# Kernel optimization log

Hardware: AMD Instinct MI355X
Metric: run time of the kernel (lower is better)

## Reference

```python
import jax, jax.numpy as jnp
import numpy as np

HEAD = 32  # HEAD_SIZE
B, T, C = 8, 1024, 768
LAYER_ID, N_LAYER = 2, 12


def wkv7(r, w, k, v, a, b):
    # RWKV7 linear recurrence (matches the custom CUDA 'attn' kernel math):
    #   S = S * exp(-exp(w)) + (S @ a) b^T + v k^T ;  y = S @ r
    Bb, Tt, Cc = r.shape
    H, N = Cc // HEAD, HEAD
    rs = lambda z: jnp.moveaxis(z.reshape(Bb, Tt, H, N), 1, 0)  # [T,B,H,N]
    rT, kT, vT, aT, bT = rs(r), rs(k), rs(v), rs(a), rs(b)
    wT = rs(jnp.exp(-jnp.exp(w)))  # decay in (0,1)
    def step(S, inp):
        rt, wt, kt, vt, at, bt = inp  # each [B,H,N]
        sa = jnp.einsum('bhij,bhj->bhi', S, at)
        S = S * wt[:, :, None, :] + sa[..., None] * bt[:, :, None, :] + vt[..., None] * kt[:, :, None, :]
        return S, jnp.einsum('bhij,bhj->bhi', S, rt)
    S0 = jnp.zeros((Bb, H, N, N), r.dtype)
    _, y = jax.lax.scan(step, S0, (rT, wT, kT, vT, aT, bT))
    return jnp.moveaxis(y, 0, 1).reshape(Bb, Tt, Cc)


def setup_inputs() -> dict:
    key = jax.random.key(0)
    ks = iter(jax.random.split(key, 64))
    def rn(shape, s=0.02):
        return (jax.random.normal(next(ks), shape, jnp.float32) * s)
    def un(shape, lim):
        return jax.random.uniform(next(ks), shape, jnp.float32, -lim, lim)
    H, N = C // HEAD, HEAD
    r10 = 1.0 - LAYER_ID / N_LAYER          # ratio_1_to_almost0
    r01 = LAYER_ID / (N_LAYER - 1)          # ratio_0_to_1
    ddd = (np.arange(C, dtype=np.float64) / C).reshape(1, 1, C)
    f32 = lambda z: jnp.asarray(z, jnp.float32)
    time_maa_x = f32(1.0 - ddd ** (0.6 * r10 ** 0.9))
    time_maa_rg = f32(1.0 - ddd ** (0.2 * r10))
    time_maa_wa = f32(1.0 - ddd ** (0.9 * r10))
    time_maa_k = f32(1.0 - (ddd ** (0.9 * r10) + 0.4 * r01))
    time_maa_v = f32(1.0 - (ddd ** (0.4 * r10) + 0.6 * r01))
    ds = -7.0 + 5.0 * (np.arange(C, dtype=np.float64) / (C - 1)) ** (0.85 + r01 ** 0.5)
    time_decay = f32(ds.reshape(1, 1, C) + 0.5)
    inp = {
        'x': jax.random.normal(next(ks), (B, T, C), jnp.float32),
        'v1': jax.random.normal(next(ks), (B, T, C), jnp.float32),
        'time_maa_x': time_maa_x, 'time_maa_rg': time_maa_rg, 'time_maa_wa': time_maa_wa,
        'time_maa_k': time_maa_k, 'time_maa_v': time_maa_v,
        'time_decay': time_decay,
        'time_faaaa': rn((1, 1, H, N), 0.05),
        'time_aaaaa': rn((1, 1, C), 0.05),
        'time_maa_w1': rn((C, 28 * 4)), 'time_maa_w2': rn((4, 28, C), 0.05),
        'time_decay_w1': rn((C, 64)), 'time_decay_w2': rn((64, C), 0.05),
        'time_aaa_w1': rn((C, 24)), 'time_aaa_w2': rn((24, C), 0.05),
        'time_kkk_w1': rn((C, 24)), 'time_kkk_w2': rn((24, C), 0.05),
        'gate_w1': rn((C, 120)), 'gate_w2': rn((120, C), 0.05),
        'ma_w1': rn((C, 24)), 'ma_w2': rn((24, C), 0.05), 'time_misc_a': rn((1, 1, C), 0.05),
        'mk_w1': rn((C, 24)), 'mk_w2': rn((24, C), 0.05), 'time_misc_k': rn((1, 1, C), 0.05),
        'mv_w1': rn((C, 24)), 'mv_w2': rn((24, C), 0.05), 'time_misc_v': 1.0 + rn((1, 1, C), 0.05),
        'Wr': un((C, C), 0.5 / C ** 0.5), 'Wk': un((C, C), 0.05 / C ** 0.5),
        'Wv': un((C, C), 0.5 / C ** 0.5), 'Wo': rn((C, C), 0.02),
        'ln_w': jnp.ones((C,), jnp.float32), 'ln_b': jnp.zeros((C,), jnp.float32),
    }
    return inp


def reference(x, v1, time_maa_x, time_maa_rg, time_maa_wa, time_maa_k, time_maa_v,
              time_decay, time_faaaa, time_aaaaa, time_maa_w1, time_maa_w2,
              time_decay_w1, time_decay_w2, time_aaa_w1, time_aaa_w2,
              time_kkk_w1, time_kkk_w2, gate_w1, gate_w2, ma_w1, ma_w2, time_misc_a,
              mk_w1, mk_w2, time_misc_k, mv_w1, mv_w2, time_misc_v,
              Wr, Wk, Wv, Wo, ln_w, ln_b):
    Bb, Tt, Cc = x.shape
    H, N = Cc // HEAD, HEAD
    # token shift: xx[t] = x[t-1] - x[t], with x[-1] = 0
    xsh = jnp.concatenate([jnp.zeros_like(x[:, :1]), x[:, :-1]], axis=1)
    xx = xsh - x
    xxx = x + xx * time_maa_x
    tm = jnp.tanh(xxx @ time_maa_w1).reshape(Bb, Tt, 4, -1)      # [B,T,4,28]
    mix = jnp.einsum('btfd,fdc->fbtc', tm, time_maa_w2)          # [4,B,T,C]
    xrg = x + xx * (time_maa_rg + mix[0])
    xwa = x + xx * (time_maa_wa + mix[1])
    xk = x + xx * (time_maa_k + mix[2])
    xv = x + xx * (time_maa_v + mix[3])
    r = xrg @ Wr
    w = -jax.nn.softplus(-(time_decay + jnp.tanh(xwa @ time_decay_w1) @ time_decay_w2)) - 0.5
    k = xk @ Wk
    v = xv @ Wv
    v = v + (v1 - v) * jax.nn.sigmoid(time_misc_v + xv @ mv_w1 @ mv_w2)
    g = jax.nn.sigmoid(xrg @ gate_w1) @ gate_w2
    kk = k + jnp.tanh(xk @ time_kkk_w1) @ time_kkk_w2
    kk4 = kk.reshape(Bb, Tt, H, N)
    nrm = jnp.maximum(jnp.sqrt(jnp.sum(kk4 * kk4, axis=-1, keepdims=True)), 1e-12)
    kk = (kk4 / nrm).reshape(Bb, Tt, Cc)
    a = jax.nn.sigmoid(time_aaaaa + xwa @ time_aaa_w1 @ time_aaa_w2)
    ma = jax.nn.sigmoid(time_misc_a + xwa @ ma_w1 @ ma_w2)
    k = k * ma + k * a * (1.0 - ma)
    mk = jax.nn.sigmoid(time_misc_k + xk @ mk_w1 @ mk_w2)
    k = k * jnp.exp(jnp.minimum(w * mk, 0.0))
    y = wkv7(r, w, k, v, -kk, kk * a)
    # GroupNorm(n_head groups) over each token, eps=6.4e-5
    yg = y.reshape(Bb, Tt, H, N)
    mu = jnp.mean(yg, axis=-1, keepdims=True)
    var = jnp.var(yg, axis=-1, keepdims=True)
    yn = (yg - mu) * jax.lax.rsqrt(var + 6.4e-05)
    yn = yn * ln_w.reshape(H, N) + ln_b.reshape(H, N)
    # per-head bonus term
    bonus = (jnp.sum(r.reshape(Bb, Tt, H, N) * k.reshape(Bb, Tt, H, N) * time_faaaa,
                     axis=-1, keepdims=True) * v.reshape(Bb, Tt, H, N))
    y = yn.reshape(Bb, Tt, Cc) + bonus.reshape(Bb, Tt, Cc)
    out = (y * g) @ Wo
    return (out, v1)
```

## Files before the change

### kernel.cpp

```cpp
#include <hip/hip_runtime.h>
#include <hip/hip_bf16.h>
#include <math.h>

#define Bdim 8
#define Tdim 1024
#define Cdim 768
#define Hdim 24
#define Ndim 32
#define BTdim (Bdim*Tdim)
#define CH6 16

typedef __attribute__((ext_vector_type(8))) short bf16x8;
typedef __attribute__((ext_vector_type(4))) float f32x4;
typedef __hip_bfloat16 bf16;

__device__ __forceinline__ float sigm(float x){ return 1.f/(1.f+expf(-x)); }
__device__ __forceinline__ float softplusf(float x){ return fmaxf(x,0.f) + log1pf(expf(-fabsf(x))); }
__device__ __forceinline__ float bf2f(bf16 v){ return __bfloat162float(v); }
__device__ __forceinline__ float us2f(unsigned short s){ return __builtin_bit_cast(float, (unsigned)s<<16); }

template<int CTRL>
__device__ __forceinline__ float dpp_add(float x){
  int xi = __builtin_bit_cast(int, x);
  int yi = __builtin_amdgcn_mov_dpp(xi, CTRL, 0xF, 0xF, true);
  return x + __builtin_bit_cast(float, yi);
}
__device__ __forceinline__ float red32(float x){
  x = dpp_add<0xB1>(x);
  x = dpp_add<0x4E>(x);
  x = dpp_add<0x141>(x);
  x = dpp_add<0x140>(x);
  x += __shfl_xor(x, 16);
  return x;
}
__device__ __forceinline__ float red16(float x){
  x = dpp_add<0xB1>(x);
  x = dpp_add<0x4E>(x);
  x = dpp_add<0x141>(x);
  x = dpp_add<0x140>(x);
  return x;
}

#define GLDS16(gp, lp) __builtin_amdgcn_global_load_lds((const __attribute__((address_space(1))) void*)(gp), (__attribute__((address_space(3))) void*)(lp), 16, 0, 0)

__global__ void k1_shift(const float* __restrict__ x, const float* __restrict__ maa_x,
                         float* __restrict__ xx, bf16* __restrict__ xxx) {
  int idx = blockIdx.x*256 + threadIdx.x;
  if (idx >= BTdim*Cdim) return;
  int c = idx % Cdim; int row = idx / Cdim; int t = row % Tdim;
  float xv = x[idx];
  float xp = (t==0) ? 0.f : x[idx - Cdim];
  float d = xp - xv;
  xx[idx] = d;
  xxx[idx] = __float2bfloat16(xv + d*maa_x[c]);
}

__global__ __launch_bounds__(256) void kconvW(const float* __restrict__ W0, const float* __restrict__ W1,
    const float* __restrict__ W2, const float* __restrict__ W3,
    bf16* __restrict__ T0, bf16* __restrict__ T1, bf16* __restrict__ T2, bf16* __restrict__ T3) {
  const float* Wsrc[4] = {W0,W1,W2,W3};
  bf16* Tdst[4] = {T0,T1,T2,T3};
  const float* W = Wsrc[blockIdx.z];
  bf16* T = Tdst[blockIdx.z];
  __shared__ float tile[32][33];
  int bx = blockIdx.x*32, by = blockIdx.y*32;
  int tx = threadIdx.x & 31, ty = threadIdx.x >> 5;
  #pragma unroll
  for (int q=0;q<32;q+=8) tile[ty+q][tx] = W[(size_t)(by+ty+q)*Cdim + bx+tx];
  __syncthreads();
  #pragma unroll
  for (int q=0;q<32;q+=8) T[(size_t)(bx+ty+q)*Cdim + by+tx] = __float2bfloat16(tile[tx][ty+q]);
}

__global__ __launch_bounds__(256) void kprep(const float* __restrict__ dw1, const float* __restrict__ aaa_w1,
    const float* __restrict__ ma_w1, const float* __restrict__ kkk_w1, const float* __restrict__ mk_w1,
    const float* __restrict__ mv_w1, const float* __restrict__ gate_w1, const float* __restrict__ maa_w1,
    const float* __restrict__ dw2, const float* __restrict__ aaa_w2, const float* __restrict__ ma_w2,
    const float* __restrict__ kkk_w2, const float* __restrict__ mk_w2, const float* __restrict__ mv_w2,
    const float* __restrict__ gate_w2,
    bf16* __restrict__ PWwa, bf16* __restrict__ PWk, bf16* __restrict__ PWv,
    bf16* __restrict__ PWrg, bf16* __restrict__ PWmaa,
    bf16* __restrict__ W2wa, bf16* __restrict__ W2k, bf16* __restrict__ W2v, bf16* __restrict__ W2g){
  int idx = blockIdx.x*256 + threadIdx.x;
  if (idx < 491520) {
    int buf = idx / 98304, rem = idx - buf*98304;
    int n = rem / 768, kk = rem - n*768;
    float val = 0.f;
    bf16* dst;
    switch(buf){
      case 0: dst=PWwa; if(n<64) val=dw1[(size_t)kk*64+n]; else if(n<88) val=aaa_w1[(size_t)kk*24+(n-64)]; else if(n<112) val=ma_w1[(size_t)kk*24+(n-88)]; break;
      case 1: dst=PWk;  if(n<24) val=kkk_w1[(size_t)kk*24+n]; else if(n<48) val=mk_w1[(size_t)kk*24+(n-24)]; break;
      case 2: dst=PWv;  if(n<24) val=mv_w1[(size_t)kk*24+n]; break;
      case 3: dst=PWrg; if(n<120) val=gate_w1[(size_t)kk*120+n]; break;
      default: dst=PWmaa; if(n<112) val=maa_w1[(size_t)kk*112+n]; break;
    }
    dst[rem] = __float2bfloat16(val);
    return;
  }
  int i = idx - 491520;
  if (i < 294912){
    int n=i>>7, q=i&127, seg=n/768, c=n-seg*768;
    float val=0.f;
    if (seg==0){ if(q<64) val=dw2[(size_t)q*768+c]; }
    else if (seg==1){ if(q>=64&&q<88) val=aaa_w2[(size_t)(q-64)*768+c]; }
    else { if(q>=88&&q<112) val=ma_w2[(size_t)(q-88)*768+c]; }
    W2wa[i]=__float2bfloat16(val); return;
  }
  i -= 294912;
  if (i < 98304){
    int n=i>>6, q=i&63, seg=n/768, c=n-seg*768;
    float val=0.f;
    if (seg==0){ if(q<24) val=kkk_w2[(size_t)q*768+c]; }
    else { if(q>=24&&q<48) val=mk_w2[(size_t)(q-24)*768+c]; }
    W2k[i]=__float2bfloat16(val); return;
  }
  i -= 98304;
  if (i < 24576){
    int c=i>>5, q=i&31;
    float val = (q<24) ? mv_w2[(size_t)q*768+c] : 0.f;
    W2v[i]=__float2bfloat16(val); return;
  }
  i -= 24576;
  if (i < 98304){
    int c=i>>7, q=i&127;
    float val = (q<120) ? gate_w2[(size_t)q*768+c] : 0.f;
    W2g[i]=__float2bfloat16(val);
  }
}

__global__ __launch_bounds__(256) void gemm_mfma(const bf16* __restrict__ A,
    const bf16* __restrict__ Bt, float* __restrict__ C, int M, int N, int K) {
  __shared__ unsigned short As[128*32];
  __shared__ unsigned short Bs[128*32];
  const int bm = blockIdx.y*128, bn = blockIdx.x*128;
  const int tid = threadIdx.x, lane = tid&63, w = tid>>6;
  const int wr = w>>1, wc = w&1;
  const int lr = lane&15, kg = lane>>4;
  f32x4 zero = {0.f,0.f,0.f,0.f};
  f32x4 acc[4][4];
  #pragma unroll
  for (int m=0;m<4;m++)
    #pragma unroll
    for (int n=0;n<4;n++) acc[m][n]=zero;
  const size_t rowA = (size_t)(bm + w*32 + (lane>>2))*K + (lane&3)*8;
  const size_t rowB = (size_t)(bn + w*32 + (lane>>2))*K + (lane&3)*8;
  unsigned short* lA = As + w*32*32;
  unsigned short* lB = Bs + w*32*32;
  for (int k0=0; k0<K; k0+=32){
    GLDS16(A + rowA + k0,                 lA);
    GLDS16(A + rowA + k0 + (size_t)16*K,  lA + 512);
    GLDS16(Bt + rowB + k0,                lB);
    GLDS16(Bt + rowB + k0 + (size_t)16*K, lB + 512);
    __syncthreads();
    bf16x8 af[4], bfr[4];
    #pragma unroll
    for (int m=0;m<4;m++) af[m]  = *(const bf16x8*)(void*)(As + (wr*64+m*16+lr)*32 + kg*8);
    #pragma unroll
    for (int n=0;n<4;n++) bfr[n] = *(const bf16x8*)(void*)(Bs + (wc*64+n*16+lr)*32 + kg*8);
    #pragma unroll
    for (int m=0;m<4;m++)
      #pragma unroll
      for (int n=0;n<4;n++)
        acc[m][n] = __builtin_amdgcn_mfma_f32_16x16x32_bf16(af[m], bfr[n], acc[m][n], 0,0,0);
    __syncthreads();
  }
  #pragma unroll
  for (int m=0;m<4;m++)
    #pragma unroll
    for (int n=0;n<4;n++){
      size_t r0 = (size_t)(bm + wr*64 + m*16 + kg*4);
      int cc = bn + wc*64 + n*16 + lr;
      #pragma unroll
      for (int q=0;q<4;q++)
        C[(r0+q)*N + cc] = acc[m][n][q];
    }
}

struct G3 {
  const bf16* A[3];
  const bf16* Bt[3];
  float* Cf[3];
  bf16* Ch[3];
  int isbf[3];
};
__global__ __launch_bounds__(256) void gemm_big3(G3 p, int N, int K) {
  const int z = blockIdx.z;
  const bf16* __restrict__ A  = p.A[z];
  const bf16* __restrict__ Bt = p.Bt[z];
  const int isbf = p.isbf[z];
  __shared__ unsigned short As[128*32];
  __shared__ unsigned short Bs[128*32];
  const int bm = blockIdx.y*128, bn = blockIdx.x*128;
  const int tid = threadIdx.x, lane = tid&63, w = tid>>6;
  const int wr = w>>1, wc = w&1;
  const int lr = lane&15, kg = lane>>4;
  f32x4 zero = {0.f,0.f,0.f,0.f};
  f32x4 acc[4][4];
  #pragma unroll
  for (int m=0;m<4;m++)
    #pragma unroll
    for (int n=0;n<4;n++) acc[m][n]=zero;
  const size_t rowA = (size_t)(bm + w*32 + (lane>>2))*K + (lane&3)*8;
  const size_t rowB = (size_t)(bn + w*32 + (lane>>2))*K + (lane&3)*8;
  unsigned short* lA = As + w*32*32;
  unsigned short* lB = Bs + w*32*32;
  for (int k0=0; k0<K; k0+=32){
    GLDS16(A + rowA + k0,                 lA);
    GLDS16(A + rowA + k0 + (size_t)16*K,  lA + 512);
    GLDS16(Bt + rowB + k0,                lB);
    GLDS16(Bt + rowB + k0 + (size_t)16*K, lB + 512);
    __syncthreads();
    bf16x8 af[4], bfr[4];
    #pragma unroll
    for (int m=0;m<4;m++) af[m]  = *(const bf16x8*)(void*)(As + (wr*64+m*16+lr)*32 + kg*8);
    #pragma unroll
    for (int n=0;n<4;n++) bfr[n] = *(const bf16x8*)(void*)(Bs + (wc*64+n*16+lr)*32 + kg*8);
    #pragma unroll
    for (int m=0;m<4;m++)
      #pragma unroll
      for (int n=0;n<4;n++)
        acc[m][n] = __builtin_amdgcn_mfma_f32_16x16x32_bf16(af[m], bfr[n], acc[m][n], 0,0,0);
    __syncthreads();
  }
  if (isbf){
    bf16* __restrict__ C = p.Ch[z];
    #pragma unroll
    for (int m=0;m<4;m++)
      #pragma unroll
      for (int n=0;n<4;n++){
        size_t r0 = (size_t)(bm + wr*64 + m*16 + kg*4);
        int cc = bn + wc*64 + n*16 + lr;
        #pragma unroll
        for (int q=0;q<4;q++)
          C[(r0+q)*N + cc] = __float2bfloat16(acc[m][n][q]);
      }
  } else {
    float* __restrict__ C = p.Cf[z];
    #pragma unroll
    for (int m=0;m<4;m++)
      #pragma unroll
      for (int n=0;n<4;n++){
        size_t r0 = (size_t)(bm + wr*64 + m*16 + kg*4);
        int cc = bn + wc*64 + n*16 + lr;
        #pragma unroll
        for (int q=0;q<4;q++)
          C[(r0+q)*N + cc] = acc[m][n][q];
      }
  }
}

__global__ __launch_bounds__(256) void gemm_tm(const bf16* __restrict__ A,
    const bf16* __restrict__ Bt, float* __restrict__ C, int K) {
  __shared__ unsigned short As[128*32];
  __shared__ unsigned short Bs[128*32];
  const int bm = blockIdx.y*128;
  const int tid = threadIdx.x, lane = tid&63, w = tid>>6;
  const int wr = w>>1, wc = w&1;
  const int lr = lane&15, kg = lane>>4;
  f32x4 zero = {0.f,0.f,0.f,0.f};
  f32x4 acc[4][4];
  #pragma unroll
  for (int m=0;m<4;m++)
    #pragma unroll
    for (int n=0;n<4;n++) acc[m][n]=zero;
  const size_t rowA = (size_t)(bm + w*32 + (lane>>2))*K + (lane&3)*8;
  const size_t rowB = (size_t)(w*32 + (lane>>2))*K + (lane&3)*8;
  unsigned short* lA = As + w*32*32;
  unsigned short* lB = Bs + w*32*32;
  for (int k0=0; k0<K; k0+=32){
    GLDS16(A + rowA + k0,                 lA);
    GLDS16(A + rowA + k0 + (size_t)16*K,  lA + 512);
    GLDS16(Bt + rowB + k0,                lB);
    GLDS16(Bt + rowB + k0 + (size_t)16*K, lB + 512);
    __syncthreads();
    bf16x8 af[4], bfr[4];
    #pragma unroll
    for (int m=0;m<4;m++) af[m]  = *(const bf16x8*)(void*)(As + (wr*64+m*16+lr)*32 + kg*8);
    #pragma unroll
    for (int n=0;n<4;n++) bfr[n] = *(const bf16x8*)(void*)(Bs + (wc*64+n*16+lr)*32 + kg*8);
    #pragma unroll
    for (int m=0;m<4;m++)
      #pragma unroll
      for (int n=0;n<4;n++)
        acc[m][n] = __builtin_amdgcn_mfma_f32_16x16x32_bf16(af[m], bfr[n], acc[m][n], 0,0,0);
    __syncthreads();
  }
  #pragma unroll
  for (int m=0;m<4;m++)
    #pragma unroll
    for (int n=0;n<4;n++){
      size_t r0 = (size_t)(bm + wr*64 + m*16 + kg*4);
      int cc = wc*64 + n*16 + lr;
      if (cc < 112){
        #pragma unroll
        for (int q=0;q<4;q++)
          C[(r0+q)*112 + cc] = tanhf(acc[m][n][q]);
      }
    }
}

struct S1P {
  const bf16* A[4];
  const bf16* Bt[4];
  bf16* C[4];
  int Ntrue[4];
  int Nalloc[4];
  int act[4];
};
__global__ __launch_bounds__(256) void gemm_s1(S1P p, int K) {
  const int z = blockIdx.z;
  const bf16* __restrict__ A  = p.A[z];
  const bf16* __restrict__ Bt = p.Bt[z];
  bf16* __restrict__ C = p.C[z];
  const int Ntrue = p.Ntrue[z], Nalloc = p.Nalloc[z], act = p.act[z];
  __shared__ unsigned short As[128*32];
  __shared__ unsigned short Bs[128*32];
  const int bm = blockIdx.y*128;
  const int tid = threadIdx.x, lane = tid&63, w = tid>>6;
  const int wr = w>>1, wc = w&1;
  const int lr = lane&15, kg = lane>>4;
  f32x4 zero = {0.f,0.f,0.f,0.f};
  f32x4 acc[4][4];
  #pragma unroll
  for (int m=0;m<4;m++)
    #pragma unroll
    for (int n=0;n<4;n++) acc[m][n]=zero;
  const size_t rowA = (size_t)(bm + w*32 + (lane>>2))*K + (lane&3)*8;
  const size_t rowB = (size_t)(w*32 + (lane>>2))*K + (lane&3)*8;
  unsigned short* lA = As + w*32*32;
  unsigned short* lB = Bs + w*32*32;
  for (int k0=0; k0<K; k0+=32){
    GLDS16(A + rowA + k0,                 lA);
    GLDS16(A + rowA + k0 + (size_t)16*K,  lA + 512);
    GLDS16(Bt + rowB + k0,                lB);
    GLDS16(Bt + rowB + k0 + (size_t)16*K, lB + 512);
    __syncthreads();
    bf16x8 af[4], bfr[4];
    #pragma unroll
    for (int m=0;m<4;m++) af[m]  = *(const bf16x8*)(void*)(As + (wr*64+m*16+lr)*32 + kg*8);
    #pragma unroll
    for (int n=0;n<4;n++) bfr[n] = *(const bf16x8*)(void*)(Bs + (wc*64+n*16+lr)*32 + kg*8);
    #pragma unroll
    for (int m=0;m<4;m++)
      #pragma unroll
      for (int n=0;n<4;n++)
        acc[m][n] = __builtin_amdgcn_mfma_f32_16x16x32_bf16(af[m], bfr[n], acc[m][n], 0,0,0);
    __syncthreads();
  }
  #pragma unroll
  for (int m=0;m<4;m++)
    #pragma unroll
    for (int n=0;n<4;n++){
      size_t r0 = (size_t)(bm + wr*64 + m*16 + kg*4);
      int cc = wc*64 + n*16 + lr;
      if (cc < Nalloc){
        #pragma unroll
        for (int q=0;q<4;q++){
          float val = acc[m][n][q];
          if      (act==1){ if (cc<64) val = tanhf(val); }
          else if (act==2){ if (cc<24) val = tanhf(val); }
          else if (act==3){ val = sigm(val); }
          if (cc >= Ntrue) val = 0.f;
          C[(r0+q)*Nalloc + cc] = __float2bfloat16(val);
        }
      }
    }
}

struct Z4 {
  const bf16* A[4];
  const bf16* Bt[4];
  bf16* C[4];
  int N[4];
  int K[4];
};
__global__ __launch_bounds__(256) void gemm_z(Z4 p) {
  const int z = blockIdx.z;
  const int N = p.N[z], K = p.K[z];
  const int bn = blockIdx.x*128;
  if (bn >= N) return;
  const bf16* __restrict__ A  = p.A[z];
  const bf16* __restrict__ Bt = p.Bt[z];
  bf16* __restrict__ C = p.C[z];
  __shared__ unsigned short As[128*32];
  __shared__ unsigned short Bs[128*32];
  const int bm = blockIdx.y*128;
  const int tid = threadIdx.x, lane = tid&63, w = tid>>6;
  const int wr = w>>1, wc = w&1;
  const int lr = lane&15, kg = lane>>4;
  f32x4 zero = {0.f,0.f,0.f,0.f};
  f32x4 acc[4][4];
  #pragma unroll
  for (int m=0;m<4;m++)
    #pragma unroll
    for (int n=0;n<4;n++) acc[m][n]=zero;
  const size_t rowA = (size_t)(bm + w*32 + (lane>>2))*K + (lane&3)*8;
  const size_t rowB = (size_t)(bn + w*32 + (lane>>2))*K + (lane&3)*8;
  unsigned short* lA = As + w*32*32;
  unsigned short* lB = Bs + w*32*32;
  for (int k0=0; k0<K; k0+=32){
    GLDS16(A + rowA + k0,                 lA);
    GLDS16(A + rowA + k0 + (size_t)16*K,  lA + 512);
    GLDS16(Bt + rowB + k0,                lB);
    GLDS16(Bt + rowB + k0 + (size_t)16*K, lB + 512);
    __syncthreads();
    bf16x8 af[4], bfr[4];
    #pragma unroll
    for (int m=0;m<4;m++) af[m]  = *(const bf16x8*)(void*)(As + (wr*64+m*16+lr)*32 + kg*8);
    #pragma unroll
    for (int n=0;n<4;n++) bfr[n] = *(const bf16x8*)(void*)(Bs + (wc*64+n*16+lr)*32 + kg*8);
    #pragma unroll
    for (int m=0;m<4;m++)
      #pragma unroll
      for (int n=0;n<4;n++)
        acc[m][n] = __builtin_amdgcn_mfma_f32_16x16x32_bf16(af[m], bfr[n], acc[m][n], 0,0,0);
    __syncthreads();
  }
  #pragma unroll
  for (int m=0;m<4;m++)
    #pragma unroll
    for (int n=0;n<4;n++){
      size_t r0 = (size_t)(bm + wr*64 + m*16 + kg*4);
      int cc = bn + wc*64 + n*16 + lr;
      #pragma unroll
      for (int q=0;q<4;q++)
        C[(r0+q)*N + cc] = __float2bfloat16(acc[m][n][q]);
    }
}

__global__ __launch_bounds__(256) void k2_mix(const float* __restrict__ x, const float* __restrict__ xx,
    const float* __restrict__ tm, const float* __restrict__ w2,
    const float* __restrict__ mrg, const float* __restrict__ mwa,
    const float* __restrict__ mk_, const float* __restrict__ mv_,
    bf16* __restrict__ xrg, bf16* __restrict__ xwa, bf16* __restrict__ xk, bf16* __restrict__ xv) {
  const int row0 = blockIdx.x*8, tid = threadIdx.x;
  __shared__ float stm[8][112];
  for (int idx=tid; idx<8*112; idx+=256){
    int rr=idx/112, q=idx-rr*112;
    stm[rr][q]=tm[(size_t)(row0+rr)*112+q];
  }
  __syncthreads();
  for (int c=tid;c<Cdim;c+=256){
    float x8[8], d8[8];
    #pragma unroll
    for (int rr=0;rr<8;rr++){
      size_t i=(size_t)(row0+rr)*Cdim+c;
      x8[rr]=x[i]; d8[rr]=xx[i];
    }
    float mrgc=mrg[c], mwac=mwa[c], mkc=mk_[c], mvc=mv_[c];
    float m0[8]={},m1[8]={},m2[8]={},m3[8]={};
    #pragma unroll 4
    for (int d=0; d<28; d++){
      float w0=w2[(size_t)(d)*Cdim + c];
      float w1=w2[(size_t)(28+d)*Cdim + c];
      float w2v=w2[(size_t)(56+d)*Cdim + c];
      float w3=w2[(size_t)(84+d)*Cdim + c];
      #pragma unroll
      for (int rr=0;rr<8;rr++){
        m0[rr]+=stm[rr][d]*w0; m1[rr]+=stm[rr][28+d]*w1;
        m2[rr]+=stm[rr][56+d]*w2v; m3[rr]+=stm[rr][84+d]*w3;
      }
    }
    #pragma unroll
    for (int rr=0;rr<8;rr++){
      size_t i=(size_t)(row0+rr)*Cdim+c;
      xrg[i]=__float2bfloat16(x8[rr] + d8[rr]*(mrgc+m0[rr]));
      xwa[i]=__float2bfloat16(x8[rr] + d8[rr]*(mwac+m1[rr]));
      xk[i] =__float2bfloat16(x8[rr] + d8[rr]*(mkc+m2[rr]));
      xv[i] =__float2bfloat16(x8[rr] + d8[rr]*(mvc+m3[rr]));
    }
  }
}

__global__ __launch_bounds__(256) void k5_fuse(
    const bf16* __restrict__ zwa, const bf16* __restrict__ zk, const bf16* __restrict__ zv,
    const float* __restrict__ td, const float* __restrict__ aaaaa,
    const float* __restrict__ misc_a, const float* __restrict__ misc_k, const float* __restrict__ misc_v,
    const float* __restrict__ v1,
    float* __restrict__ kbuf, float* __restrict__ vbuf, float* __restrict__ wexp,
    bf16* __restrict__ kb_bf, bf16* __restrict__ vb_bf,
    bf16* __restrict__ akv, bf16* __restrict__ bkv) {
  const int row = blockIdx.x, tid = threadIdx.x;
  float kraw[3], v0[3], v1v[3];
  #pragma unroll
  for (int it=0;it<3;it++){
    size_t i=(size_t)row*Cdim + tid + it*256;
    kraw[it]=kbuf[i]; v0[it]=vbuf[i]; v1v[it]=v1[i];
  }
  __syncthreads();
  #pragma unroll
  for (int it=0;it<3;it++){
    const int c = tid + it*256;
    const size_t i=(size_t)row*Cdim+c;
    float zd = bf2f(zwa[(size_t)row*2304 + c]);
    float za = bf2f(zwa[(size_t)row*2304 + 768 + c]);
    float zma= bf2f(zwa[(size_t)row*2304 + 1536 + c]);
    float zkk= bf2f(zk[(size_t)row*1536 + c]);
    float zmk= bf2f(zk[(size_t)row*1536 + 768 + c]);
    float zmv= bf2f(zv[i]);
    float w = -softplusf(-(td[c]+zd)) - 0.5f;
    wexp[i] = expf(-expf(w));
    float a  = sigm(aaaaa[c]+za);
    float ma = sigm(misc_a[c]+zma);
    float mk = sigm(misc_k[c]+zmk);
    float mv = sigm(misc_v[c]+zmv);
    vb_bf[i] = __float2bfloat16(v0[it] + (v1v[it]-v0[it])*mv);
    float kf = kraw[it]*(ma + a*(1.f-ma))*expf(fminf(w*mk,0.f));
    kb_bf[i] = __float2bfloat16(kf);
    float kk = kraw[it] + zkk;
    float ss = red32(kk*kk);
    float kkn = kk * (1.f/fmaxf(sqrtf(ss),1e-12f));
    akv[i] = __float2bfloat16(-kkn);
    bkv[i] = __float2bfloat16(kkn*a);
  }
}

struct TReg { unsigned r,k,a,b; float2 w; unsigned short v; };
__global__ __launch_bounds__(64) void k6_wkv(const unsigned short* __restrict__ r, const float* __restrict__ wd,
    const unsigned short* __restrict__ k, const unsigned short* __restrict__ v,
    const unsigned short* __restrict__ a, const unsigned short* __restrict__ b2, float* __restrict__ y) {
  const int lane = threadIdx.x;
  const int bid = blockIdx.x;
  const int head = bid % (Bdim*Hdim);
  const int rq   = bid / (Bdim*Hdim);
  const int bb = head / Hdim, hh = head - bb*Hdim;
  const int i0 = rq*4 + (lane >> 4);
  const int jh = lane & 15;
  const int col = jh*2;
  __shared__ __align__(16) float swd[2][CH6][Ndim];
  __shared__ __align__(16) unsigned short sbf[2][4][CH6][Ndim];
  __shared__ __align__(16) unsigned short sv2[2][CH6][Ndim];
  const unsigned short* gb16[4] = {r, k, a, b2};
  const size_t gbase = (size_t)bb*Tdim*Cdim + (size_t)hh*Ndim;
  float S0=0.f, S1=0.f;

  auto STAGE = [&](int c, int buf){
    const size_t tb = (size_t)c*CH6;
    GLDS16(wd + gbase + (tb +   (lane>>3))*Cdim + (lane&7)*4, &swd[buf][0][0]);
    GLDS16(wd + gbase + (tb + 8+(lane>>3))*Cdim + (lane&7)*4, &swd[buf][8][0]);
    #pragma unroll
    for (int arr=0; arr<4; arr++)
      GLDS16(gb16[arr] + gbase + (tb + (lane>>2))*Cdim + (lane&3)*8, &sbf[buf][arr][0][0]);
    GLDS16(v + gbase + (tb + (lane>>2))*Cdim + (lane&3)*8, &sv2[buf][0][0]);
  };

  auto LOADT = [&](TReg& d, int buf, int t){
    d.r = *(const unsigned*)&sbf[buf][0][t][col];
    d.k = *(const unsigned*)&sbf[buf][1][t][col];
    d.a = *(const unsigned*)&sbf[buf][2][t][col];
    d.b = *(const unsigned*)&sbf[buf][3][t][col];
    d.w = *(const float2*)&swd[buf][t][col];
    d.v = sv2[buf][t][i0];
  };

  STAGE(0, 0);
  asm volatile("s_waitcnt vmcnt(0)" ::: "memory");
  TReg pA, pB;
  LOADT(pA, 0, 0);
  LOADT(pB, 0, 1);
  int buf = 0;
  const int NCH = Tdim/CH6;
  for (int c=0; c<NCH; ++c){
    if (c+1 < NCH) STAGE(c+1, buf^1);
    const size_t yb = gbase + (size_t)c*CH6*Cdim;
    #pragma unroll
    for (int t=0; t<CH6; t++){
      TReg& cur = (t&1) ? pB : pA;
      const unsigned cr=cur.r, ck=cur.k, ca=cur.a, cb=cur.b;
      const float2 cw=cur.w;
      const unsigned short cv=cur.v;
      const int tt = t+2;
      if (tt < CH6) {
        LOADT(cur, buf, tt);
      } else if (c+1 < NCH) {
        if (tt == CH6) asm volatile("s_waitcnt vmcnt(0)" ::: "memory");
        LOADT(cur, buf^1, tt-CH6);
      }
      float a0 = __builtin_bit_cast(float, ca<<16);
      float a1 = __builtin_bit_cast(float, ca&0xFFFF0000u);
      float sa = S0*a0 + S1*a1;
      sa = red16(sa);
      float k0 = __builtin_bit_cast(float, ck<<16);
      float k1 = __builtin_bit_cast(float, ck&0xFFFF0000u);
      float b0 = __builtin_bit_cast(float, cb<<16);
      float b1 = __builtin_bit_cast(float, cb&0xFFFF0000u);
      float r0 = __builtin_bit_cast(float, cr<<16);
      float r1 = __builtin_bit_cast(float, cr&0xFFFF0000u);
      const float vl = us2f(cv);
      S0 = S0*cw.x + (sa*b0 + vl*k0);
      S1 = S1*cw.y + (sa*b1 + vl*k1);
      float yv = S0*r0 + S1*r1;
      yv = red16(yv);
      if (jh == 0) y[yb + (size_t)t*Cdim + i0] = yv;
    }
    buf ^= 1;
  }
}

__global__ __launch_bounds__(256) void k7_post(const float* __restrict__ y,
    const bf16* __restrict__ r, const bf16* __restrict__ kf, const bf16* __restrict__ v,
    const bf16* __restrict__ g, const float* __restrict__ faaaa,
    const float* __restrict__ lnw, const float* __restrict__ lnb,
    bf16* __restrict__ ygate,
    const float4* __restrict__ v1c, float4* __restrict__ outc) {
  const int row = blockIdx.x, tid = threadIdx.x;
  if (tid < 192) outc[(size_t)row*192 + tid] = v1c[(size_t)row*192 + tid];
  #pragma unroll
  for (int it=0; it<3; it++){
    const int c = tid + it*256;
    const size_t i = (size_t)row*Cdim + c;
    float yv = y[i];
    float bon = bf2f(r[i])*bf2f(kf[i])*faaaa[c];
    float s  = red32(yv);
    float ss = red32(yv*yv);
    float bn = red32(bon);
    float mu = s*(1.f/Ndim);
    float var = ss*(1.f/Ndim) - mu*mu;
    float rs = rsqrtf(var + 6.4e-5f);
    float yn = (yv-mu)*rs*lnw[c]+lnb[c];
    ygate[i]=__float2bfloat16((yn + bn*bf2f(v[i]))*bf2f(g[i]));
  }
}

extern "C" void kernel_launch(void* const* d_in, const int* in_sizes, int n_in,
                              void* d_out, int out_size, void* d_ws, size_t ws_size,
                              hipStream_t stream) {
  const float* x      = (const float*)d_in[0];
  const float* v1     = (const float*)d_in[1];
  const float* maa_x  = (const float*)d_in[2];
  const float* maa_rg = (const float*)d_in[3];
  const float* maa_wa = (const float*)d_in[4];
  const float* maa_k  = (const float*)d_in[5];
  const float* maa_v  = (const float*)d_in[6];
  const float* time_decay = (const float*)d_in[7];
  const float* faaaa  = (const float*)d_in[8];
  const float* aaaaa  = (const float*)d_in[9];
  const float* maa_w1 = (const float*)d_in[10];
  const float* maa_w2 = (const float*)d_in[11];
  const float* dw1    = (const float*)d_in[12];
  const float* dw2    = (const float*)d_in[13];
  const float* aaa_w1 = (const float*)d_in[14];
  const float* aaa_w2 = (const float*)d_in[15];
  const float* kkk_w1 = (const float*)d_in[16];
  const float* kkk_w2 = (const float*)d_in[17];
  const float* gate_w1= (const float*)d_in[18];
  const float* gate_w2= (const float*)d_in[19];
  const float* ma_w1  = (const float*)d_in[20];
  const float* ma_w2  = (const float*)d_in[21];
  const float* misc_a = (const float*)d_in[22];
  const float* mk_w1  = (const float*)d_in[23];
  const float* mk_w2  = (const float*)d_in[24];
  const float* misc_k = (const float*)d_in[25];
  const float* mv_w1  = (const float*)d_in[26];
  const float* mv_w2  = (const float*)d_in[27];
  const float* misc_v = (const float*)d_in[28];
  const float* Wr     = (const float*)d_in[29];
  const float* Wk     = (const float*)d_in[30];
  const float* Wv     = (const float*)d_in[31];
  const float* Wo     = (const float*)d_in[32];
  const float* lnw    = (const float*)d_in[33];
  const float* lnb    = (const float*)d_in[34];
  float* out = (float*)d_out;

  float* ws = (float*)d_ws;
  const size_t BTC = (size_t)BTdim*Cdim;
  const size_t HB  = BTC/2;
  float* xx   = ws;                float* wexp = ws;
  float* kb   = ws + 2*HB;         bf16* kb_bf = (bf16*)kb;
  float* vb   = ws + 4*HB;         bf16* vb_bf = (bf16*)vb;
  bf16* xrg_bf = (bf16*)(ws + 6*HB);
  bf16* xwa_bf = xrg_bf + BTC;
  bf16* zwa_bf = (bf16*)(ws + 6*HB);
  bf16* xk_bf  = (bf16*)(ws + 9*HB);
  bf16* xv_bf  = xk_bf + BTC;
  bf16* zk_bf  = (bf16*)(ws + 9*HB);
  bf16* xxx_bf = (bf16*)(ws + 11*HB);
  bf16* zv_bf  = (bf16*)(ws + 11*HB);
  float* tm    = ws + 12*HB;
  bf16* zg_bf  = (bf16*)(ws + 12*HB);
  bf16* hwa_bf = (bf16*)(ws + 13*HB);
  bf16* hk_bf  = hwa_bf + (size_t)BTdim*128;
  bf16* hv_bf  = hk_bf  + (size_t)BTdim*64;
  bf16* hrg_bf = hv_bf  + (size_t)BTdim*32;
  bf16* akv_bf = (bf16*)(ws + 13*HB);
  bf16* bkv_bf = (bf16*)(ws + 14*HB);
  bf16* yg_bf  = (bf16*)(ws + 14*HB);
  float* ybuf  = ws + 15*HB;
  bf16* rb_bf  = (bf16*)(ws + 17*HB);
  bf16* Wbase  = (bf16*)(ws + 18*HB);
  bf16* WtR = Wbase;
  bf16* WtK = WtR + 589824;
  bf16* WtV = WtK + 589824;
  bf16* WtO = WtV + 589824;
  bf16* PWwa = WtO + 589824;
  bf16* PWk  = PWwa + 98304;
  bf16* PWv  = PWk  + 98304;
  bf16* PWrg = PWv  + 98304;
  bf16* PWmaa= PWrg + 98304;
  bf16* W2wa = PWmaa + 98304;
  bf16* W2k  = W2wa + 294912;
  bf16* W2v  = W2k  + 98304;
  bf16* W2g  = W2v  + 24576;

  dim3 blk(256);
  kconvW<<<dim3(24,24,4), blk, 0, stream>>>(Wr,Wk,Wv,Wo, WtR,WtK,WtV,WtO);
  kprep<<<dim3(3936), blk, 0, stream>>>(dw1,aaa_w1,ma_w1,kkk_w1,mk_w1,mv_w1,gate_w1,maa_w1,
                                        dw2,aaa_w2,ma_w2,kkk_w2,mk_w2,mv_w2,gate_w2,
                                        PWwa,PWk,PWv,PWrg,PWmaa, W2wa,W2k,W2v,W2g);
  k1_shift<<<dim3((BTdim*Cdim+255)/256), blk, 0, stream>>>(x, maa_x, xx, xxx_bf);
  gemm_tm<<<dim3(1,64), blk, 0, stream>>>(xxx_bf, PWmaa, tm, Cdim);
  k2_mix<<<dim3(BTdim/8), blk, 0, stream>>>(x, xx, tm, maa_w2, maa_rg, maa_wa, maa_k, maa_v,
                                            xrg_bf, xwa_bf, xk_bf, xv_bf);
  {
    S1P p{};
    p.A[0]=xwa_bf; p.Bt[0]=PWwa; p.C[0]=hwa_bf; p.Ntrue[0]=112; p.Nalloc[0]=128; p.act[0]=1;
    p.A[1]=xk_bf;  p.Bt[1]=PWk;  p.C[1]=hk_bf;  p.Ntrue[1]=48;  p.Nalloc[1]=64;  p.act[1]=2;
    p.A[2]=xv_bf;  p.Bt[2]=PWv;  p.C[2]=hv_bf;  p.Ntrue[2]=24;  p.Nalloc[2]=32;  p.act[2]=0;
    p.A[3]=xrg_bf; p.Bt[3]=PWrg; p.C[3]=hrg_bf; p.Ntrue[3]=120; p.Nalloc[3]=128; p.act[3]=3;
    gemm_s1<<<dim3(1,64,4), blk, 0, stream>>>(p, Cdim);
  }
  {
    G3 p{};
    p.A[0]=xrg_bf; p.Bt[0]=WtR; p.Ch[0]=rb_bf; p.Cf[0]=nullptr; p.isbf[0]=1;
    p.A[1]=xk_bf;  p.Bt[1]=WtK; p.Cf[1]=kb;    p.Ch[1]=nullptr; p.isbf[1]=0;
    p.A[2]=xv_bf;  p.Bt[2]=WtV; p.Cf[2]=vb;    p.Ch[2]=nullptr; p.isbf[2]=0;
    gemm_big3<<<dim3(6,64,3), blk, 0, stream>>>(p, Cdim, Cdim);
  }
  {
    Z4 p{};
    p.A[0]=hwa_bf; p.Bt[0]=W2wa; p.C[0]=zwa_bf; p.N[0]=2304; p.K[0]=128;
    p.A[1]=hk_bf;  p.Bt[1]=W2k;  p.C[1]=zk_bf;  p.N[1]=1536; p.K[1]=64;
    p.A[2]=hv_bf;  p.Bt[2]=W2v;  p.C[2]=zv_bf;  p.N[2]=768;  p.K[2]=32;
    p.A[3]=hrg_bf; p.Bt[3]=W2g;  p.C[3]=zg_bf;  p.N[3]=768;  p.K[3]=128;
    gemm_z<<<dim3(18,64,4), blk, 0, stream>>>(p);
  }
  k5_fuse<<<dim3(BTdim), blk, 0, stream>>>(zwa_bf, zk_bf, zv_bf,
      time_decay, aaaaa, misc_a, misc_k, misc_v, v1,
      kb, vb, wexp, kb_bf, vb_bf, akv_bf, bkv_bf);
  k6_wkv<<<dim3(Bdim*Hdim*8), dim3(64), 0, stream>>>((const unsigned short*)rb_bf, wexp,
      (const unsigned short*)kb_bf, (const unsigned short*)vb_bf,
      (const unsigned short*)akv_bf, (const unsigned short*)bkv_bf, ybuf);
  k7_post<<<dim3(BTdim), blk, 0, stream>>>(ybuf, rb_bf, kb_bf, vb_bf, zg_bf, faaaa, lnw, lnb, yg_bf,
                                           (const float4*)v1, (float4*)(out + BTC));
  gemm_mfma<<<dim3(6,64), blk, 0, stream>>>(yg_bf, WtO, out, BTdim, Cdim, Cdim);
}
```

Baseline: 527.1 us.

## Interleave r/k/a/b per head, bf16 intermediates, one-column-per-lane WKV recurrence

The k and v projection GEMMs now write bf16 instead of fp32, and k5 packs r, k, a and b into one head-interleaved buffer so each WKV timestep needs a single 8-byte load per lane. The WKV kernel now gives each lane one state element, with two rows per wave instead of four, and launches twice as many blocks. It uses 8-step chunks and writes y in bf16, which k7 then reads. This cuts memory traffic and gives the serial recurrence more parallelism, at the cost of a full 32-lane reduction (including a cross-row shuffle) per step and lower precision in y, k and v.

```diff
diff --git a/kernel.cpp b/kernel.cpp
--- a/kernel.cpp
+++ b/kernel.cpp
@@ -8,7 +8,6 @@
 #define Hdim 24
 #define Ndim 32
 #define BTdim (Bdim*Tdim)
-#define CH6 16
 
 typedef __attribute__((ext_vector_type(8))) short bf16x8;
 typedef __attribute__((ext_vector_type(4))) float f32x4;
@@ -31,13 +30,6 @@
   x = dpp_add<0x141>(x);
   x = dpp_add<0x140>(x);
   x += __shfl_xor(x, 16);
-  return x;
-}
-__device__ __forceinline__ float red16(float x){
-  x = dpp_add<0xB1>(x);
-  x = dpp_add<0x4E>(x);
-  x = dpp_add<0x141>(x);
-  x = dpp_add<0x140>(x);
   return x;
 }
 
@@ -179,15 +171,13 @@
 struct G3 {
   const bf16* A[3];
   const bf16* Bt[3];
-  float* Cf[3];
-  bf16* Ch[3];
-  int isbf[3];
+  bf16* C[3];
 };
 __global__ __launch_bounds__(256) void gemm_big3(G3 p, int N, int K) {
   const int z = blockIdx.z;
   const bf16* __restrict__ A  = p.A[z];
   const bf16* __restrict__ Bt = p.Bt[z];
-  const int isbf = p.isbf[z];
+  bf16* __restrict__ C = p.C[z];
   __shared__ unsigned short As[128*32];
   __shared__ unsigned short Bs[128*32];
   const int bm = blockIdx.y*128, bn = blockIdx.x*128;
@@ -222,31 +212,16 @@
         acc[m][n] = __builtin_amdgcn_mfma_f32_16x16x32_bf16(af[m], bfr[n], acc[m][n], 0,0,0);
     __syncthreads();
   }
-  if (isbf){
-    bf16* __restrict__ C = p.Ch[z];
-    #pragma unroll
-    for (int m=0;m<4;m++)
-      #pragma unroll
-      for (int n=0;n<4;n++){
-        size_t r0 = (size_t)(bm + wr*64 + m*16 + kg*4);
-        int cc = bn + wc*64 + n*16 + lr;
-        #pragma unroll
-        for (int q=0;q<4;q++)
-          C[(r0+q)*N + cc] = __float2bfloat16(acc[m][n][q]);
-      }
-  } else {
-    float* __restrict__ C = p.Cf[z];
-    #pragma unroll
-    for (int m=0;m<4;m++)
-      #pragma unroll
-      for (int n=0;n<4;n++){
-        size_t r0 = (size_t)(bm + wr*64 + m*16 + kg*4);
-        int cc = bn + wc*64 + n*16 + lr;
-        #pragma unroll
-        for (int q=0;q<4;q++)
-          C[(r0+q)*N + cc] = acc[m][n][q];
-      }
-  }
+  #pragma unroll
+  for (int m=0;m<4;m++)
+    #pragma unroll
+    for (int n=0;n<4;n++){
+      size_t r0 = (size_t)(bm + wr*64 + m*16 + kg*4);
+      int cc = bn + wc*64 + n*16 + lr;
+      #pragma unroll
+      for (int q=0;q<4;q++)
+        C[(r0+q)*N + cc] = __float2bfloat16(acc[m][n][q]);
+    }
 }
 
 __global__ __launch_bounds__(256) void gemm_tm(const bf16* __restrict__ A,
@@ -474,24 +449,18 @@
 
 __global__ __launch_bounds__(256) void k5_fuse(
     const bf16* __restrict__ zwa, const bf16* __restrict__ zk, const bf16* __restrict__ zv,
+    const bf16* __restrict__ rbf, const bf16* __restrict__ kbf, bf16* __restrict__ vbf,
     const float* __restrict__ td, const float* __restrict__ aaaaa,
     const float* __restrict__ misc_a, const float* __restrict__ misc_k, const float* __restrict__ misc_v,
     const float* __restrict__ v1,
-    float* __restrict__ kbuf, float* __restrict__ vbuf, float* __restrict__ wexp,
-    bf16* __restrict__ kb_bf, bf16* __restrict__ vb_bf,
-    bf16* __restrict__ akv, bf16* __restrict__ bkv) {
+    float* __restrict__ wexp, unsigned short* __restrict__ rkab) {
   const int row = blockIdx.x, tid = threadIdx.x;
-  float kraw[3], v0[3], v1v[3];
-  #pragma unroll
-  for (int it=0;it<3;it++){
-    size_t i=(size_t)row*Cdim + tid + it*256;
-    kraw[it]=kbuf[i]; v0[it]=vbuf[i]; v1v[it]=v1[i];
-  }
-  __syncthreads();
   #pragma unroll
   for (int it=0;it<3;it++){
     const int c = tid + it*256;
-    const size_t i=(size_t)row*Cdim+c;
+    const size_t i = (size_t)row*Cdim + c;
+    float kraw = bf2f(kbf[i]);
+    float v0   = bf2f(vbf[i]);
     float zd = bf2f(zwa[(size_t)row*2304 + c]);
     float za = bf2f(zwa[(size_t)row*2304 + 768 + c]);
     float zma= bf2f(zwa[(size_t)row*2304 + 1536 + c]);
@@ -504,101 +473,94 @@
     float ma = sigm(misc_a[c]+zma);
     float mk = sigm(misc_k[c]+zmk);
     float mv = sigm(misc_v[c]+zmv);
-    vb_bf[i] = __float2bfloat16(v0[it] + (v1v[it]-v0[it])*mv);
-    float kf = kraw[it]*(ma + a*(1.f-ma))*expf(fminf(w*mk,0.f));
-    kb_bf[i] = __float2bfloat16(kf);
-    float kk = kraw[it] + zkk;
+    vbf[i] = __float2bfloat16(v0 + (v1[i]-v0)*mv);
+    float kf = kraw*(ma + a*(1.f-ma))*expf(fminf(w*mk,0.f));
+    float kk = kraw + zkk;
     float ss = red32(kk*kk);
     float kkn = kk * (1.f/fmaxf(sqrtf(ss),1e-12f));
-    akv[i] = __float2bfloat16(-kkn);
-    bkv[i] = __float2bfloat16(kkn*a);
-  }
-}
-
-struct TReg { unsigned r,k,a,b; float2 w; unsigned short v; };
-__global__ __launch_bounds__(64) void k6_wkv(const unsigned short* __restrict__ r, const float* __restrict__ wd,
-    const unsigned short* __restrict__ k, const unsigned short* __restrict__ v,
-    const unsigned short* __restrict__ a, const unsigned short* __restrict__ b2, float* __restrict__ y) {
+    unsigned rus = (unsigned)__builtin_bit_cast(unsigned short, rbf[i]);
+    unsigned kus = (unsigned)__builtin_bit_cast(unsigned short, __float2bfloat16(kf));
+    unsigned aus = (unsigned)__builtin_bit_cast(unsigned short, __float2bfloat16(-kkn));
+    unsigned bus = (unsigned)__builtin_bit_cast(unsigned short, __float2bfloat16(kkn*a));
+    uint2 pk;
+    pk.x = rus | (kus<<16);
+    pk.y = aus | (bus<<16);
+    *(uint2*)&rkab[((size_t)row*Hdim + (c>>5))*128 + (size_t)(c&31)*4] = pk;
+  }
+}
+
+struct TR { uint2 g; float w; unsigned short v; };
+__global__ __launch_bounds__(64) void k6_wkv(const unsigned short* __restrict__ rkab,
+    const float* __restrict__ wd, const unsigned short* __restrict__ vbf, bf16* __restrict__ y) {
   const int lane = threadIdx.x;
   const int bid = blockIdx.x;
   const int head = bid % (Bdim*Hdim);
   const int rq   = bid / (Bdim*Hdim);
   const int bb = head / Hdim, hh = head - bb*Hdim;
-  const int i0 = rq*4 + (lane >> 4);
-  const int jh = lane & 15;
-  const int col = jh*2;
-  __shared__ __align__(16) float swd[2][CH6][Ndim];
-  __shared__ __align__(16) unsigned short sbf[2][4][CH6][Ndim];
-  __shared__ __align__(16) unsigned short sv2[2][CH6][Ndim];
-  const unsigned short* gb16[4] = {r, k, a, b2};
-  const size_t gbase = (size_t)bb*Tdim*Cdim + (size_t)hh*Ndim;
-  float S0=0.f, S1=0.f;
-
+  const int i0 = rq*2 + (lane>>5);
+  const int j  = lane & 31;
+  __shared__ __align__(16) unsigned short srk[2][8][128];
+  __shared__ __align__(16) float sw[2][8][32];
+  __shared__ __align__(16) unsigned short sv[2][2][8][32];
+  const size_t wvbase = (size_t)bb*Tdim*Cdim + (size_t)hh*Ndim;
+  float S = 0.f;
+
+  auto rkrow = [&](size_t t){ return (((size_t)bb*Tdim + t)*Hdim + hh)*128; };
   auto STAGE = [&](int c, int buf){
-    const size_t tb = (size_t)c*CH6;
-    GLDS16(wd + gbase + (tb +   (lane>>3))*Cdim + (lane&7)*4, &swd[buf][0][0]);
-    GLDS16(wd + gbase + (tb + 8+(lane>>3))*Cdim + (lane&7)*4, &swd[buf][8][0]);
-    #pragma unroll
-    for (int arr=0; arr<4; arr++)
-      GLDS16(gb16[arr] + gbase + (tb + (lane>>2))*Cdim + (lane&3)*8, &sbf[buf][arr][0][0]);
-    GLDS16(v + gbase + (tb + (lane>>2))*Cdim + (lane&3)*8, &sv2[buf][0][0]);
+    const size_t tb = (size_t)c*8;
+    GLDS16(rkab + rkrow(tb +     (lane>>4)) + (size_t)(lane&15)*8, &srk[buf][0][0]);
+    GLDS16(rkab + rkrow(tb + 4 + (lane>>4)) + (size_t)(lane&15)*8, &srk[buf][4][0]);
+    GLDS16(wd + wvbase + (tb + (lane>>3))*Cdim + (lane&7)*4, &sw[buf][0][0]);
+    { int h = lane&31;
+      GLDS16(vbf + wvbase + (tb + (h>>2))*Cdim + (h&3)*8, &sv[buf][0][0][0]); }
   };
-
-  auto LOADT = [&](TReg& d, int buf, int t){
-    d.r = *(const unsigned*)&sbf[buf][0][t][col];
-    d.k = *(const unsigned*)&sbf[buf][1][t][col];
-    d.a = *(const unsigned*)&sbf[buf][2][t][col];
-    d.b = *(const unsigned*)&sbf[buf][3][t][col];
-    d.w = *(const float2*)&swd[buf][t][col];
-    d.v = sv2[buf][t][i0];
+  auto LOADT = [&](TR& d, int buf, int t){
+    d.g = *(const uint2*)&srk[buf][t][j*4];
+    d.w = sw[buf][t][j];
+    d.v = sv[buf][0][t][i0];
   };
 
   STAGE(0, 0);
   asm volatile("s_waitcnt vmcnt(0)" ::: "memory");
-  TReg pA, pB;
+  TR pA, pB;
   LOADT(pA, 0, 0);
   LOADT(pB, 0, 1);
   int buf = 0;
-  const int NCH = Tdim/CH6;
+  const int NCH = Tdim/8;
   for (int c=0; c<NCH; ++c){
     if (c+1 < NCH) STAGE(c+1, buf^1);
-    const size_t yb = gbase + (size_t)c*CH6*Cdim;
-    #pragma unroll
-    for (int t=0; t<CH6; t++){
-      TReg& cur = (t&1) ? pB : pA;
-      const unsigned cr=cur.r, ck=cur.k, ca=cur.a, cb=cur.b;
-      const float2 cw=cur.w;
-      const unsigned short cv=cur.v;
+    const size_t yb = wvbase + (size_t)c*8*Cdim;
+    #pragma unroll
+    for (int t=0; t<8; t++){
+      TR& cur = (t&1) ? pB : pA;
+      const uint2 g = cur.g;
+      const float wv = cur.w;
+      const unsigned short vv = cur.v;
       const int tt = t+2;
-      if (tt < CH6) {
+      if (tt < 8) {
         LOADT(cur, buf, tt);
       } else if (c+1 < NCH) {
-        if (tt == CH6) asm volatile("s_waitcnt vmcnt(0)" ::: "memory");
-        LOADT(cur, buf^1, tt-CH6);
+        if (tt == 8) asm volatile("s_waitcnt vmcnt(0)" ::: "memory");
+        LOADT(cur, buf^1, tt-8);
       }
-      float a0 = __builtin_bit_cast(float, ca<<16);
-      float a1 = __builtin_bit_cast(float, ca&0xFFFF0000u);
-      float sa = S0*a0 + S1*a1;
-      sa = red16(sa);
-      float k0 = __builtin_bit_cast(float, ck<<16);
-      float k1 = __builtin_bit_cast(float, ck&0xFFFF0000u);
-      float b0 = __builtin_bit_cast(float, cb<<16);
-      float b1 = __builtin_bit_cast(float, cb&0xFFFF0000u);
-      float r0 = __builtin_bit_cast(float, cr<<16);
-      float r1 = __builtin_bit_cast(float, cr&0xFFFF0000u);
-      const float vl = us2f(cv);
-      S0 = S0*cw.x + (sa*b0 + vl*k0);
-      S1 = S1*cw.y + (sa*b1 + vl*k1);
-      float yv = S0*r0 + S1*r1;
-      yv = red16(yv);
-      if (jh == 0) y[yb + (size_t)t*Cdim + i0] = yv;
+      float rf = __builtin_bit_cast(float, g.x<<16);
+      float kf = __builtin_bit_cast(float, g.x & 0xFFFF0000u);
+      float af = __builtin_bit_cast(float, g.y<<16);
+      float bv = __builtin_bit_cast(float, g.y & 0xFFFF0000u);
+      float vl = us2f(vv);
+      float sa = S*af;
+      sa = red32(sa);
+      S = S*wv + (sa*bv + vl*kf);
+      float yv = S*rf;
+      yv = red32(yv);
+      if (j == 0) y[yb + (size_t)t*Cdim + i0] = __float2bfloat16(yv);
     }
     buf ^= 1;
   }
 }
 
-__global__ __launch_bounds__(256) void k7_post(const float* __restrict__ y,
-    const bf16* __restrict__ r, const bf16* __restrict__ kf, const bf16* __restrict__ v,
+__global__ __launch_bounds__(256) void k7_post(const bf16* __restrict__ y,
+    const unsigned short* __restrict__ rkab, const bf16* __restrict__ v,
     const bf16* __restrict__ g, const float* __restrict__ faaaa,
     const float* __restrict__ lnw, const float* __restrict__ lnb,
     bf16* __restrict__ ygate,
@@ -609,8 +571,11 @@
   for (int it=0; it<3; it++){
     const int c = tid + it*256;
     const size_t i = (size_t)row*Cdim + c;
-    float yv = y[i];
-    float bon = bf2f(r[i])*bf2f(kf[i])*faaaa[c];
+    float yv = bf2f(y[i]);
+    unsigned rk = *(const unsigned*)&rkab[((size_t)row*Hdim + (c>>5))*128 + (size_t)(c&31)*4];
+    float rf = __builtin_bit_cast(float, rk<<16);
+    float kf = __builtin_bit_cast(float, rk & 0xFFFF0000u);
+    float bon = rf*kf*faaaa[c];
     float s  = red32(yv);
     float ss = red32(yv*yv);
     float bn = red32(bon);
@@ -665,28 +630,28 @@
   float* ws = (float*)d_ws;
   const size_t BTC = (size_t)BTdim*Cdim;
   const size_t HB  = BTC/2;
-  float* xx   = ws;                float* wexp = ws;
-  float* kb   = ws + 2*HB;         bf16* kb_bf = (bf16*)kb;
-  float* vb   = ws + 4*HB;         bf16* vb_bf = (bf16*)vb;
-  bf16* xrg_bf = (bf16*)(ws + 6*HB);
+  float* xx    = ws;
+  float* wexp  = ws;
+  bf16* kb_bf  = (bf16*)(ws + 2*HB);
+  bf16* ybuf_bf= (bf16*)(ws + 2*HB);
+  bf16* vb_bf  = (bf16*)(ws + 3*HB);
+  bf16* xrg_bf = (bf16*)(ws + 4*HB);
   bf16* xwa_bf = xrg_bf + BTC;
-  bf16* zwa_bf = (bf16*)(ws + 6*HB);
-  bf16* xk_bf  = (bf16*)(ws + 9*HB);
+  bf16* zwa_bf = (bf16*)(ws + 4*HB);
+  bf16* xk_bf  = (bf16*)(ws + 7*HB);
   bf16* xv_bf  = xk_bf + BTC;
-  bf16* zk_bf  = (bf16*)(ws + 9*HB);
-  bf16* xxx_bf = (bf16*)(ws + 11*HB);
-  bf16* zv_bf  = (bf16*)(ws + 11*HB);
-  float* tm    = ws + 12*HB;
-  bf16* zg_bf  = (bf16*)(ws + 12*HB);
-  bf16* hwa_bf = (bf16*)(ws + 13*HB);
+  bf16* zk_bf  = (bf16*)(ws + 7*HB);
+  bf16* xxx_bf = (bf16*)(ws + 9*HB);
+  bf16* zv_bf  = (bf16*)(ws + 9*HB);
+  float* tm    = ws + 10*HB;
+  bf16* zg_bf  = (bf16*)(ws + 10*HB);
+  bf16* hwa_bf = (bf16*)(ws + 11*HB);
   bf16* hk_bf  = hwa_bf + (size_t)BTdim*128;
   bf16* hv_bf  = hk_bf  + (size_t)BTdim*64;
   bf16* hrg_bf = hv_bf  + (size_t)BTdim*32;
-  bf16* akv_bf = (bf16*)(ws + 13*HB);
-  bf16* bkv_bf = (bf16*)(ws + 14*HB);
-  bf16* yg_bf  = (bf16*)(ws + 14*HB);
-  float* ybuf  = ws + 15*HB;
-  bf16* rb_bf  = (bf16*)(ws + 17*HB);
+  unsigned short* rkab = (unsigned short*)(ws + 12*HB);
+  bf16* rb_bf  = (bf16*)(ws + 16*HB);
+  bf16* yg_bf  = (bf16*)(ws + 17*HB);
   bf16* Wbase  = (bf16*)(ws + 18*HB);
   bf16* WtR = Wbase;
   bf16* WtK = WtR + 589824;
@@ -721,9 +686,9 @@
   }
   {
     G3 p{};
-    p.A[0]=xrg_bf; p.Bt[0]=WtR; p.Ch[0]=rb_bf; p.Cf[0]=nullptr; p.isbf[0]=1;
-    p.A[1]=xk_bf;  p.Bt[1]=WtK; p.Cf[1]=kb;    p.Ch[1]=nullptr; p.isbf[1]=0;
-    p.A[2]=xv_bf;  p.Bt[2]=WtV; p.Cf[2]=vb;    p.Ch[2]=nullptr; p.isbf[2]=0;
+    p.A[0]=xrg_bf; p.Bt[0]=WtR; p.C[0]=rb_bf;
+    p.A[1]=xk_bf;  p.Bt[1]=WtK; p.C[1]=kb_bf;
+    p.A[2]=xv_bf;  p.Bt[2]=WtV; p.C[2]=vb_bf;
     gemm_big3<<<dim3(6,64,3), blk, 0, stream>>>(p, Cdim, Cdim);
   }
   {
@@ -734,13 +699,11 @@
     p.A[3]=hrg_bf; p.Bt[3]=W2g;  p.C[3]=zg_bf;  p.N[3]=768;  p.K[3]=128;
     gemm_z<<<dim3(18,64,4), blk, 0, stream>>>(p);
   }
-  k5_fuse<<<dim3(BTdim), blk, 0, stream>>>(zwa_bf, zk_bf, zv_bf,
-      time_decay, aaaaa, misc_a, misc_k, misc_v, v1,
-      kb, vb, wexp, kb_bf, vb_bf, akv_bf, bkv_bf);
-  k6_wkv<<<dim3(Bdim*Hdim*8), dim3(64), 0, stream>>>((const unsigned short*)rb_bf, wexp,
-      (const unsigned short*)kb_bf, (const unsigned short*)vb_bf,
-      (const unsigned short*)akv_bf, (const unsigned short*)bkv_bf, ybuf);
-  k7_post<<<dim3(BTdim), blk, 0, stream>>>(ybuf, rb_bf, kb_bf, vb_bf, zg_bf, faaaa, lnw, lnb, yg_bf,
+  k5_fuse<<<dim3(BTdim), blk, 0, stream>>>(zwa_bf, zk_bf, zv_bf, rb_bf, kb_bf, vb_bf,
+      time_decay, aaaaa, misc_a, misc_k, misc_v, v1, wexp, rkab);
+  k6_wkv<<<dim3(Bdim*Hdim*16), dim3(64), 0, stream>>>(rkab, wexp,
+      (const unsigned short*)vb_bf, ybuf_bf);
+  k7_post<<<dim3(BTdim), blk, 0, stream>>>(ybuf_bf, rkab, vb_bf, zg_bf, faaaa, lnw, lnb, yg_bf,
                                            (const float4*)v1, (float4*)(out + BTC));
   gemm_mfma<<<dim3(6,64), blk, 0, stream>>>(yg_bf, WtO, out, BTdim, Cdim, Cdim);
 }
```

New measurement: 618.0 us. 1.17x slower.
